# Performance work log

Measured on AMD Instinct MI355X. Metric: run time of the kernel, lower is better.

The kernel has to match this reference:

```python
import jax, jax.numpy as jnp
import numpy as np

N = 50000
E = 800000
D_IN = 128
D_H = 128
D_OUT = 128
EPS = 1e-5


def setup_inputs() -> dict:
    key = jax.random.key(0)
    ks = jax.random.split(key, 16)
    s = 1.0 / np.sqrt(D_IN)
    inp = {
        "x": jax.random.normal(ks[0], (N, D_IN), dtype=jnp.float32),
        "src": jax.random.randint(ks[1], (E,), 0, N, dtype=jnp.int32),
        "dst": jax.random.randint(ks[2], (E,), 0, N, dtype=jnp.int32),
        # SAGEConv layer 1 (in->hidden): fc_self, fc_neigh, bias
        "Ws1": jax.random.uniform(ks[3], (D_IN, D_H), jnp.float32, -s, s),
        "Wn1": jax.random.uniform(ks[4], (D_IN, D_H), jnp.float32, -s, s),
        "b1": jnp.zeros((D_H,), jnp.float32),
        # BN1
        "gamma1": jnp.ones((D_H,), jnp.float32),
        "beta1": jnp.zeros((D_H,), jnp.float32),
        # SAGEConv layer 2 (hidden->hidden)
        "Ws2": jax.random.uniform(ks[5], (D_H, D_H), jnp.float32, -s, s),
        "Wn2": jax.random.uniform(ks[6], (D_H, D_H), jnp.float32, -s, s),
        "b2": jnp.zeros((D_H,), jnp.float32),
        # BN2
        "gamma2": jnp.ones((D_H,), jnp.float32),
        "beta2": jnp.zeros((D_H,), jnp.float32),
        # SAGEConv layer 3 (hidden->out)
        "Ws3": jax.random.uniform(ks[7], (D_H, D_OUT), jnp.float32, -s, s),
        "Wn3": jax.random.uniform(ks[8], (D_H, D_OUT), jnp.float32, -s, s),
        "b3": jnp.zeros((D_OUT,), jnp.float32),
    }
    return inp


def _sage_conv(x, src, dst, Ws, Wn, b):
    # mean aggregation of neighbor (src) features onto dst nodes
    agg = jax.ops.segment_sum(x[src], dst, num_segments=N)  # [N, d]
    deg = jax.ops.segment_sum(jnp.ones((E,), x.dtype), dst, num_segments=N)
    h_neigh = agg / jnp.maximum(deg, 1.0)[:, None]  # isolated nodes -> 0
    return x @ Ws + h_neigh @ Wn + b


def _batch_norm(h, gamma, beta):
    mu = jnp.mean(h, axis=0)
    var = jnp.mean(jnp.square(h - mu), axis=0)  # biased var (torch BN)
    return (h - mu) * jax.lax.rsqrt(var + EPS) * gamma + beta


def reference(x, src, dst, Ws1, Wn1, b1, gamma1, beta1,
              Ws2, Wn2, b2, gamma2, beta2, Ws3, Wn3, b3):
    h = jax.nn.relu(_batch_norm(_sage_conv(x, src, dst, Ws1, Wn1, b1), gamma1, beta1))
    # dropout is identity at inference
    h = jax.nn.relu(_batch_norm(_sage_conv(h, src, dst, Ws2, Wn2, b2), gamma2, beta2))
    return _sage_conv(h, src, dst, Ws3, Wn3, b3)
```

## Files before the change

### kernel.cpp

```cpp
#include <hip/hip_runtime.h>

#define N_NODES 50000
#define NEDGE   800000
#define D       128
#define EPS     1e-5f

typedef __attribute__((ext_vector_type(8))) short bf16x8;
typedef __attribute__((ext_vector_type(4))) float f32x4;
typedef __attribute__((ext_vector_type(8))) unsigned short u16x8;

__device__ inline uint32_t bfhi(float f) {
    uint32_t u = __float_as_uint(f);
    u += 0x7fffu + ((u >> 16) & 1u);
    return u >> 16;
}
__device__ inline float bff(uint32_t h) { return __uint_as_float(h << 16); }

__global__ __launch_bounds__(256) void k_deg(const int* __restrict__ dst,
                                             int* __restrict__ degi) {
    int e = blockIdx.x * 256 + threadIdx.x;
    if (e < NEDGE) atomicAdd(&degi[dst[e]], 1);
}

__global__ __launch_bounds__(256) void k_scan1(const int* __restrict__ degi,
                                               int* __restrict__ offs,
                                               int* __restrict__ bsum) {
    __shared__ int s[256];
    int tid = threadIdx.x;
    int i = blockIdx.x * 256 + tid;
    int v = (i < N_NODES) ? degi[i] : 0;
    s[tid] = v;
    __syncthreads();
    for (int d = 1; d < 256; d <<= 1) {
        int t = (tid >= d) ? s[tid - d] : 0;
        __syncthreads();
        s[tid] += t;
        __syncthreads();
    }
    if (i < N_NODES) offs[i] = s[tid] - v;
    if (tid == 255) bsum[blockIdx.x] = s[255];
}

__global__ __launch_bounds__(256) void k_scan2(int* __restrict__ bsum, int nb) {
    __shared__ int s[256];
    int tid = threadIdx.x;
    int v = (tid < nb) ? bsum[tid] : 0;
    s[tid] = v;
    __syncthreads();
    for (int d = 1; d < 256; d <<= 1) {
        int t = (tid >= d) ? s[tid - d] : 0;
        __syncthreads();
        s[tid] += t;
        __syncthreads();
    }
    if (tid < nb) bsum[tid] = s[tid] - v;
}

__global__ __launch_bounds__(256) void k_scan3(const int* __restrict__ degi,
                                               const int* __restrict__ bsum,
                                               int* __restrict__ offs,
                                               int* __restrict__ cursor,
                                               float* __restrict__ invdeg) {
    int i = blockIdx.x * 256 + threadIdx.x;
    if (i < N_NODES) {
        int o = offs[i] + bsum[blockIdx.x];
        offs[i] = o;
        cursor[i] = o;
        int dg = degi[i];
        invdeg[i] = 1.0f / (float)(dg > 0 ? dg : 1);
    }
    if (i == 0 && blockIdx.x == 0) offs[N_NODES] = NEDGE;
}

__global__ __launch_bounds__(256) void k_fill(const int* __restrict__ src,
                                              const int* __restrict__ dst,
                                              int* __restrict__ cursor,
                                              int* __restrict__ csr) {
    int e = blockIdx.x * 256 + threadIdx.x;
    if (e < NEDGE) {
        int p = atomicAdd(&cursor[dst[e]], 1);
        csr[p] = src[e];
    }
}

__global__ __launch_bounds__(256) void k_tobf16(const float* __restrict__ X,
                                                unsigned short* __restrict__ XB) {
    int t = blockIdx.x * 256 + threadIdx.x;
    if (t >= (N_NODES * D) / 8) return;
    const float* p = X + (size_t)t * 8;
    float4 a = *reinterpret_cast<const float4*>(p);
    float4 b = *reinterpret_cast<const float4*>(p + 4);
    u16x8 o;
    o[0] = (unsigned short)bfhi(a.x); o[1] = (unsigned short)bfhi(a.y);
    o[2] = (unsigned short)bfhi(a.z); o[3] = (unsigned short)bfhi(a.w);
    o[4] = (unsigned short)bfhi(b.x); o[5] = (unsigned short)bfhi(b.y);
    o[6] = (unsigned short)bfhi(b.z); o[7] = (unsigned short)bfhi(b.w);
    *reinterpret_cast<u16x8*>(XB + (size_t)t * 8) = o;
}

__global__ __launch_bounds__(256) void k_agg(const unsigned short* __restrict__ XB,
                                             const int* __restrict__ offs,
                                             const int* __restrict__ csr,
                                             const float* __restrict__ invdeg,
                                             const float* __restrict__ bnscale,
                                             const float* __restrict__ bnshift,
                                             int useBn,
                                             float* __restrict__ HN) {
    int n = blockIdx.x * 16 + (threadIdx.x >> 4);
    if (n >= N_NODES) return;
    int c = (threadIdx.x & 15) * 8;

    float sc[8], sh[8];
    if (useBn) {
        float4 s0 = *reinterpret_cast<const float4*>(bnscale + c);
        float4 s1 = *reinterpret_cast<const float4*>(bnscale + c + 4);
        float4 h0 = *reinterpret_cast<const float4*>(bnshift + c);
        float4 h1 = *reinterpret_cast<const float4*>(bnshift + c + 4);
        sc[0] = s0.x; sc[1] = s0.y; sc[2] = s0.z; sc[3] = s0.w;
        sc[4] = s1.x; sc[5] = s1.y; sc[6] = s1.z; sc[7] = s1.w;
        sh[0] = h0.x; sh[1] = h0.y; sh[2] = h0.z; sh[3] = h0.w;
        sh[4] = h1.x; sh[5] = h1.y; sh[6] = h1.z; sh[7] = h1.w;
    }

    int e0 = offs[n], e1 = offs[n + 1];
    float acc[8];
#pragma unroll
    for (int i = 0; i < 8; ++i) acc[i] = 0.f;

    for (int e = e0; e < e1; ++e) {
        int s = csr[e];
        u16x8 v = *reinterpret_cast<const u16x8*>(XB + (size_t)s * D + c);
        if (useBn) {
#pragma unroll
            for (int i = 0; i < 8; ++i)
                acc[i] += fmaxf(bff((unsigned short)v[i]) * sc[i] + sh[i], 0.f);
        } else {
#pragma unroll
            for (int i = 0; i < 8; ++i)
                acc[i] += bff((unsigned short)v[i]);
        }
    }
    float id = invdeg[n];
    float4 o0 = {acc[0] * id, acc[1] * id, acc[2] * id, acc[3] * id};
    float4 o1 = {acc[4] * id, acc[5] * id, acc[6] * id, acc[7] * id};
    *reinterpret_cast<float4*>(HN + (size_t)n * D + c) = o0;
    *reinterpret_cast<float4*>(HN + (size_t)n * D + c + 4) = o1;
}

__global__ __launch_bounds__(256) void k_wprep(const float* __restrict__ W0,
                                               const float* __restrict__ W1,
                                               const float* __restrict__ W2,
                                               const float* __restrict__ W3,
                                               const float* __restrict__ W4,
                                               const float* __restrict__ W5,
                                               unsigned short* __restrict__ wt) {
    int mat = blockIdx.x >> 6;
    const float* srcs[6] = {W0, W1, W2, W3, W4, W5};
    const float* W = srcs[mat];
    int t = (blockIdx.x & 63) * 256 + threadIdx.x;
    int k = t >> 7;
    int n = t & 127;
    float w = W[k * 128 + n];
    uint32_t h = bfhi(w);
    uint32_t l = bfhi(w - bff(h));
    unsigned short* base = wt + (size_t)mat * 32768;
    base[n * 128 + k] = (unsigned short)h;
    base[16384 + n * 128 + k] = (unsigned short)l;
}

#define LDS_RS 272
#define LDS_PLANE (64 * LDS_RS)
__global__ __launch_bounds__(512) void k_mm(const float* __restrict__ Xf,
                                            const unsigned short* __restrict__ Xhi,
                                            const unsigned short* __restrict__ Xlo,
                                            const float* __restrict__ HN,
                                            const unsigned short* __restrict__ WsT,
                                            const unsigned short* __restrict__ WnT,
                                            const float* __restrict__ bias,
                                            const float* __restrict__ bnscale,
                                            const float* __restrict__ bnshift,
                                            int mode,
                                            float* __restrict__ OUTf,
                                            unsigned short* __restrict__ OUThi,
                                            unsigned short* __restrict__ OUTlo,
                                            int outFp32,
                                            int doStats,
                                            float* __restrict__ sums) {
    __shared__ __align__(16) unsigned char smem[4 * LDS_PLANE];

    const int tid = threadIdx.x;
    const int lane = tid & 63;
    const int wave = tid >> 6;
    const int row0 = blockIdx.x * 64;
    const int mlo = lane & 15;
    const int g = lane >> 4;
    const int col = (wave << 4) + mlo;
    const int kb = g * 8;

    bf16x8 wsh[4], wsl[4], wnh[4], wnl[4];
#pragma unroll
    for (int kc = 0; kc < 4; ++kc) {
        int ko = kc * 32 + kb;
        wsh[kc] = *reinterpret_cast<const bf16x8*>(WsT + (size_t)col * 128 + ko);
        wsl[kc] = *reinterpret_cast<const bf16x8*>(WsT + 16384 + (size_t)col * 128 + ko);
        wnh[kc] = *reinterpret_cast<const bf16x8*>(WnT + (size_t)col * 128 + ko);
        wnl[kc] = *reinterpret_cast<const bf16x8*>(WnT + 16384 + (size_t)col * 128 + ko);
    }

#pragma unroll
    for (int uu = 0; uu < 2; ++uu) {
        int u = tid + uu * 512;
        int r = u >> 4;
        int ks = u & 15;
        int grow = row0 + r;
        float f[8], a[8];
        if (grow < N_NODES) {
            if (mode == 0) {
                const float* xp = Xf + (size_t)grow * D + ks * 8;
                float4 x0 = *reinterpret_cast<const float4*>(xp);
                float4 x1 = *reinterpret_cast<const float4*>(xp + 4);
                f[0] = x0.x; f[1] = x0.y; f[2] = x0.z; f[3] = x0.w;
                f[4] = x1.x; f[5] = x1.y; f[6] = x1.z; f[7] = x1.w;
            } else {
                u16x8 hi = *reinterpret_cast<const u16x8*>(Xhi + (size_t)grow * D + ks * 8);
                u16x8 lo = *reinterpret_cast<const u16x8*>(Xlo + (size_t)grow * D + ks * 8);
                float4 s0 = *reinterpret_cast<const float4*>(bnscale + ks * 8);
                float4 s1 = *reinterpret_cast<const float4*>(bnscale + ks * 8 + 4);
                float4 h0 = *reinterpret_cast<const float4*>(bnshift + ks * 8);
                float4 h1 = *reinterpret_cast<const float4*>(bnshift + ks * 8 + 4);
                float scv[8] = {s0.x, s0.y, s0.z, s0.w, s1.x, s1.y, s1.z, s1.w};
                float shv[8] = {h0.x, h0.y, h0.z, h0.w, h1.x, h1.y, h1.z, h1.w};
#pragma unroll
                for (int i = 0; i < 8; ++i) {
                    float v = bff((unsigned short)hi[i]) + bff((unsigned short)lo[i]);
                    f[i] = fmaxf(v * scv[i] + shv[i], 0.f);
                }
            }
            const float* ap = HN + (size_t)grow * D + ks * 8;
            float4 a0 = *reinterpret_cast<const float4*>(ap);
            float4 a1 = *reinterpret_cast<const float4*>(ap + 4);
            a[0] = a0.x; a[1] = a0.y; a[2] = a0.z; a[3] = a0.w;
            a[4] = a1.x; a[5] = a1.y; a[6] = a1.z; a[7] = a1.w;
        } else {
#pragma unroll
            for (int i = 0; i < 8; ++i) { f[i] = 0.f; a[i] = 0.f; }
        }
        int base = r * LDS_RS + ks * 16;
        uint32_t h8[8];
        int4 vhi, vlo;
#pragma unroll
        for (int i = 0; i < 8; ++i) h8[i] = bfhi(f[i]);
        vhi.x = h8[0] | (h8[1] << 16); vhi.y = h8[2] | (h8[3] << 16);
        vhi.z = h8[4] | (h8[5] << 16); vhi.w = h8[6] | (h8[7] << 16);
        {
            uint32_t l0 = bfhi(f[0] - bff(h8[0])), l1 = bfhi(f[1] - bff(h8[1]));
            uint32_t l2 = bfhi(f[2] - bff(h8[2])), l3 = bfhi(f[3] - bff(h8[3]));
            uint32_t l4 = bfhi(f[4] - bff(h8[4])), l5 = bfhi(f[5] - bff(h8[5]));
            uint32_t l6 = bfhi(f[6] - bff(h8[6])), l7 = bfhi(f[7] - bff(h8[7]));
            vlo.x = l0 | (l1 << 16); vlo.y = l2 | (l3 << 16);
            vlo.z = l4 | (l5 << 16); vlo.w = l6 | (l7 << 16);
        }
        *reinterpret_cast<int4*>(smem + 0 * LDS_PLANE + base) = vhi;
        *reinterpret_cast<int4*>(smem + 1 * LDS_PLANE + base) = vlo;
#pragma unroll
        for (int i = 0; i < 8; ++i) h8[i] = bfhi(a[i]);
        vhi.x = h8[0] | (h8[1] << 16); vhi.y = h8[2] | (h8[3] << 16);
        vhi.z = h8[4] | (h8[5] << 16); vhi.w = h8[6] | (h8[7] << 16);
        {
            uint32_t l0 = bfhi(a[0] - bff(h8[0])), l1 = bfhi(a[1] - bff(h8[1]));
            uint32_t l2 = bfhi(a[2] - bff(h8[2])), l3 = bfhi(a[3] - bff(h8[3]));
            uint32_t l4 = bfhi(a[4] - bff(h8[4])), l5 = bfhi(a[5] - bff(h8[5]));
            uint32_t l6 = bfhi(a[6] - bff(h8[6])), l7 = bfhi(a[7] - bff(h8[7]));
            vlo.x = l0 | (l1 << 16); vlo.y = l2 | (l3 << 16);
            vlo.z = l4 | (l5 << 16); vlo.w = l6 | (l7 << 16);
        }
        *reinterpret_cast<int4*>(smem + 2 * LDS_PLANE + base) = vhi;
        *reinterpret_cast<int4*>(smem + 3 * LDS_PLANE + base) = vlo;
    }
    __syncthreads();

    f32x4 acc[4];
#pragma unroll
    for (int s = 0; s < 4; ++s) acc[s] = (f32x4){0.f, 0.f, 0.f, 0.f};

#pragma unroll
    for (int kc = 0; kc < 4; ++kc) {
        int ksr = kc * 4 + g;
        int ko = ksr * 16;
#pragma unroll
        for (int s = 0; s < 4; ++s) {
            int ad = (s * 16 + mlo) * LDS_RS + ko;
            bf16x8 xh = *reinterpret_cast<const bf16x8*>(smem + 0 * LDS_PLANE + ad);
            bf16x8 xl = *reinterpret_cast<const bf16x8*>(smem + 1 * LDS_PLANE + ad);
            bf16x8 ah = *reinterpret_cast<const bf16x8*>(smem + 2 * LDS_PLANE + ad);
            bf16x8 al = *reinterpret_cast<const bf16x8*>(smem + 3 * LDS_PLANE + ad);
            acc[s] = __builtin_amdgcn_mfma_f32_16x16x32_bf16(xh, wsh[kc], acc[s], 0, 0, 0);
            acc[s] = __builtin_amdgcn_mfma_f32_16x16x32_bf16(xh, wsl[kc], acc[s], 0, 0, 0);
            acc[s] = __builtin_amdgcn_mfma_f32_16x16x32_bf16(xl, wsh[kc], acc[s], 0, 0, 0);
            acc[s] = __builtin_amdgcn_mfma_f32_16x16x32_bf16(ah, wnh[kc], acc[s], 0, 0, 0);
            acc[s] = __builtin_amdgcn_mfma_f32_16x16x32_bf16(ah, wnl[kc], acc[s], 0, 0, 0);
            acc[s] = __builtin_amdgcn_mfma_f32_16x16x32_bf16(al, wnh[kc], acc[s], 0, 0, 0);
        }
    }

    float bcol = bias[col];
    float cs = 0.f, cq = 0.f;
#pragma unroll
    for (int s = 0; s < 4; ++s) {
#pragma unroll
        for (int r = 0; r < 4; ++r) {
            int grow = row0 + s * 16 + g * 4 + r;
            if (grow < N_NODES) {
                float v = acc[s][r] + bcol;
                if (outFp32) {
                    OUTf[(size_t)grow * D + col] = v;
                } else {
                    uint32_t h = bfhi(v);
                    OUThi[(size_t)grow * D + col] = (unsigned short)h;
                    OUTlo[(size_t)grow * D + col] = (unsigned short)bfhi(v - bff(h));
                }
                cs += v; cq += v * v;
            }
        }
    }
    if (doStats) {
        cs += __shfl_xor(cs, 16); cs += __shfl_xor(cs, 32);
        cq += __shfl_xor(cq, 16); cq += __shfl_xor(cq, 32);
        if (lane < 16) {
            atomicAdd(&sums[col], cs);
            atomicAdd(&sums[128 + col], cq);
        }
    }
}

__global__ void k_bnfin(const float* __restrict__ sums,
                        const float* __restrict__ gamma,
                        const float* __restrict__ beta,
                        float* __restrict__ scale,
                        float* __restrict__ shift) {
    int c = threadIdx.x;
    const float invN = 1.0f / (float)N_NODES;
    float mu = sums[c] * invN;
    float var = sums[128 + c] * invN - mu * mu;
    float s = gamma[c] * rsqrtf(var + EPS);
    scale[c] = s;
    shift[c] = beta[c] - mu * s;
}

extern "C" void kernel_launch(void* const* d_in, const int* in_sizes, int n_in,
                              void* d_out, int out_size, void* d_ws, size_t ws_size,
                              hipStream_t stream) {
    const float* x   = (const float*)d_in[0];
    const int*   src = (const int*)d_in[1];
    const int*   dst = (const int*)d_in[2];
    const float* Ws1 = (const float*)d_in[3];
    const float* Wn1 = (const float*)d_in[4];
    const float* b1  = (const float*)d_in[5];
    const float* g1  = (const float*)d_in[6];
    const float* be1 = (const float*)d_in[7];
    const float* Ws2 = (const float*)d_in[8];
    const float* Wn2 = (const float*)d_in[9];
    const float* b2  = (const float*)d_in[10];
    const float* g2  = (const float*)d_in[11];
    const float* be2 = (const float*)d_in[12];
    const float* Ws3 = (const float*)d_in[13];
    const float* Wn3 = (const float*)d_in[14];
    const float* b3  = (const float*)d_in[15];
    float* out = (float*)d_out;

    char* p = (char*)d_ws;
    auto alloc = [&](size_t bytes) -> char* {
        char* r = p;
        p += (bytes + 255) & ~(size_t)255;
        return r;
    };
    float* hn   = (float*)alloc((size_t)N_NODES * D * 4);
    unsigned short* xb   = (unsigned short*)alloc((size_t)N_NODES * D * 2);
    unsigned short* h1hi = (unsigned short*)alloc((size_t)N_NODES * D * 2);
    unsigned short* h1lo = (unsigned short*)alloc((size_t)N_NODES * D * 2);
    unsigned short* h2hi = (unsigned short*)alloc((size_t)N_NODES * D * 2);
    unsigned short* h2lo = (unsigned short*)alloc((size_t)N_NODES * D * 2);
    int*   csr    = (int*)alloc((size_t)NEDGE * 4);
    int*   offs   = (int*)alloc((size_t)(N_NODES + 1) * 4);
    int*   cursor = (int*)alloc((size_t)N_NODES * 4);
    int*   degi   = (int*)alloc((size_t)N_NODES * 4);
    float* invdeg = (float*)alloc((size_t)N_NODES * 4);
    int*   bsum   = (int*)alloc(1024);
    float* sums   = (float*)alloc(256 * 4);
    float* scale  = (float*)alloc(128 * 4);
    float* shift  = (float*)alloc(128 * 4);
    unsigned short* wt = (unsigned short*)alloc((size_t)6 * 32768 * 2);

    const int NB_E = (NEDGE + 255) / 256;
    const int NB_N = (N_NODES + 255) / 256;
    const int NB_A = (N_NODES + 15) / 16;
    const int NB_M = (N_NODES + 63) / 64;
    const int NB_T = (N_NODES * D / 8 + 255) / 256;

    const unsigned short* WsT1 = wt + 0 * 32768;
    const unsigned short* WnT1 = wt + 1 * 32768;
    const unsigned short* WsT2 = wt + 2 * 32768;
    const unsigned short* WnT2 = wt + 3 * 32768;
    const unsigned short* WsT3 = wt + 4 * 32768;
    const unsigned short* WnT3 = wt + 5 * 32768;

    k_wprep<<<384, 256, 0, stream>>>(Ws1, Wn1, Ws2, Wn2, Ws3, Wn3, wt);
    hipMemsetAsync(degi, 0, (size_t)N_NODES * 4, stream);
    k_deg<<<NB_E, 256, 0, stream>>>(dst, degi);
    k_scan1<<<NB_N, 256, 0, stream>>>(degi, offs, bsum);
    k_scan2<<<1, 256, 0, stream>>>(bsum, NB_N);
    k_scan3<<<NB_N, 256, 0, stream>>>(degi, bsum, offs, cursor, invdeg);
    k_fill<<<NB_E, 256, 0, stream>>>(src, dst, cursor, csr);
    k_tobf16<<<NB_T, 256, 0, stream>>>(x, xb);

    k_agg<<<NB_A, 256, 0, stream>>>(xb, offs, csr, invdeg, scale, shift, 0, hn);
    hipMemsetAsync(sums, 0, 256 * 4, stream);
    k_mm<<<NB_M, 512, 0, stream>>>(x, h1hi, h1lo, hn, WsT1, WnT1, b1, scale, shift,
                                   0, out, h1hi, h1lo, 0, 1, sums);
    k_bnfin<<<1, 128, 0, stream>>>(sums, g1, be1, scale, shift);

    k_agg<<<NB_A, 256, 0, stream>>>(h1hi, offs, csr, invdeg, scale, shift, 1, hn);
    hipMemsetAsync(sums, 0, 256 * 4, stream);
    k_mm<<<NB_M, 512, 0, stream>>>(x, h1hi, h1lo, hn, WsT2, WnT2, b2, scale, shift,
                                   1, out, h2hi, h2lo, 0, 1, sums);
    k_bnfin<<<1, 128, 0, stream>>>(sums, g2, be2, scale, shift);

    k_agg<<<NB_A, 256, 0, stream>>>(h2hi, offs, csr, invdeg, scale, shift, 1, hn);
    k_mm<<<NB_M, 512, 0, stream>>>(x, h2hi, h2lo, hn, WsT3, WnT3, b3, scale, shift,
                                   1, out, h1hi, h1lo, 1, 0, sums);
}
```

Measured before the change: 441.0 us.

## Restructure matmul into persistent multi-tile blocks with register prefetch and swizzled LDS

The dense matmul kernel now uses 256-thread blocks that each process three 32-row tiles. Each wave covers two 16-column groups, the weights stay in registers across tiles, and the next tile's global loads are prefetched into registers while the current tile is on the MFMA units. The LDS layout switches from padded rows to an XOR swizzle to avoid bank conflicts. The aggregation loop is also unrolled by two with dual accumulators to keep more gathers in flight. The cost is higher register pressure and extra barriers per tile.

```diff
diff --git a/kernel.cpp b/kernel.cpp
--- a/kernel.cpp
+++ b/kernel.cpp
@@ -4,6 +4,10 @@
 #define NEDGE   800000
 #define D       128
 #define EPS     1e-5f
+#define MTILE   32
+#define TPB_TILES 3
+#define NTILES  1563
+#define NB_MM   521
 
 typedef __attribute__((ext_vector_type(8))) short bf16x8;
 typedef __attribute__((ext_vector_type(4))) float f32x4;
@@ -123,26 +127,47 @@
     }
 
     int e0 = offs[n], e1 = offs[n + 1];
-    float acc[8];
-#pragma unroll
-    for (int i = 0; i < 8; ++i) acc[i] = 0.f;
-
-    for (int e = e0; e < e1; ++e) {
-        int s = csr[e];
-        u16x8 v = *reinterpret_cast<const u16x8*>(XB + (size_t)s * D + c);
+    float a0[8], a1[8];
+#pragma unroll
+    for (int i = 0; i < 8; ++i) { a0[i] = 0.f; a1[i] = 0.f; }
+
+    int e = e0;
+    for (; e + 2 <= e1; e += 2) {
+        int s0i = csr[e], s1i = csr[e + 1];
+        u16x8 v0 = *reinterpret_cast<const u16x8*>(XB + (size_t)s0i * D + c);
+        u16x8 v1 = *reinterpret_cast<const u16x8*>(XB + (size_t)s1i * D + c);
         if (useBn) {
 #pragma unroll
+            for (int i = 0; i < 8; ++i) {
+                a0[i] += fmaxf(bff((unsigned short)v0[i]) * sc[i] + sh[i], 0.f);
+                a1[i] += fmaxf(bff((unsigned short)v1[i]) * sc[i] + sh[i], 0.f);
+            }
+        } else {
+#pragma unroll
+            for (int i = 0; i < 8; ++i) {
+                a0[i] += bff((unsigned short)v0[i]);
+                a1[i] += bff((unsigned short)v1[i]);
+            }
+        }
+    }
+    if (e < e1) {
+        int s0i = csr[e];
+        u16x8 v0 = *reinterpret_cast<const u16x8*>(XB + (size_t)s0i * D + c);
+        if (useBn) {
+#pragma unroll
             for (int i = 0; i < 8; ++i)
-                acc[i] += fmaxf(bff((unsigned short)v[i]) * sc[i] + sh[i], 0.f);
+                a0[i] += fmaxf(bff((unsigned short)v0[i]) * sc[i] + sh[i], 0.f);
         } else {
 #pragma unroll
             for (int i = 0; i < 8; ++i)
-                acc[i] += bff((unsigned short)v[i]);
+                a0[i] += bff((unsigned short)v0[i]);
         }
     }
     float id = invdeg[n];
-    float4 o0 = {acc[0] * id, acc[1] * id, acc[2] * id, acc[3] * id};
-    float4 o1 = {acc[4] * id, acc[5] * id, acc[6] * id, acc[7] * id};
+    float4 o0 = {(a0[0] + a1[0]) * id, (a0[1] + a1[1]) * id,
+                 (a0[2] + a1[2]) * id, (a0[3] + a1[3]) * id};
+    float4 o1 = {(a0[4] + a1[4]) * id, (a0[5] + a1[5]) * id,
+                 (a0[6] + a1[6]) * id, (a0[7] + a1[7]) * id};
     *reinterpret_cast<float4*>(HN + (size_t)n * D + c) = o0;
     *reinterpret_cast<float4*>(HN + (size_t)n * D + c + 4) = o1;
 }
@@ -168,167 +193,222 @@
     base[16384 + n * 128 + k] = (unsigned short)l;
 }
 
-#define LDS_RS 272
-#define LDS_PLANE (64 * LDS_RS)
-__global__ __launch_bounds__(512) void k_mm(const float* __restrict__ Xf,
-                                            const unsigned short* __restrict__ Xhi,
-                                            const unsigned short* __restrict__ Xlo,
-                                            const float* __restrict__ HN,
-                                            const unsigned short* __restrict__ WsT,
-                                            const unsigned short* __restrict__ WnT,
-                                            const float* __restrict__ bias,
-                                            const float* __restrict__ bnscale,
-                                            const float* __restrict__ bnshift,
-                                            int mode,
-                                            float* __restrict__ OUTf,
-                                            unsigned short* __restrict__ OUThi,
-                                            unsigned short* __restrict__ OUTlo,
-                                            int outFp32,
-                                            int doStats,
-                                            float* __restrict__ sums) {
-    __shared__ __align__(16) unsigned char smem[4 * LDS_PLANE];
+__global__ __launch_bounds__(256, 2) void k_mm(const float* __restrict__ Xf,
+                                               const unsigned short* __restrict__ Xhi,
+                                               const unsigned short* __restrict__ Xlo,
+                                               const float* __restrict__ HN,
+                                               const unsigned short* __restrict__ WsT,
+                                               const unsigned short* __restrict__ WnT,
+                                               const float* __restrict__ bias,
+                                               const float* __restrict__ bnscale,
+                                               const float* __restrict__ bnshift,
+                                               int mode,
+                                               float* __restrict__ OUTf,
+                                               unsigned short* __restrict__ OUThi,
+                                               unsigned short* __restrict__ OUTlo,
+                                               int outFp32,
+                                               int doStats,
+                                               float* __restrict__ sums) {
+    __shared__ __align__(16) unsigned char smem[4 * 8192];
 
     const int tid = threadIdx.x;
     const int lane = tid & 63;
     const int wave = tid >> 6;
-    const int row0 = blockIdx.x * 64;
     const int mlo = lane & 15;
     const int g = lane >> 4;
-    const int col = (wave << 4) + mlo;
-    const int kb = g * 8;
-
-    bf16x8 wsh[4], wsl[4], wnh[4], wnl[4];
-#pragma unroll
-    for (int kc = 0; kc < 4; ++kc) {
-        int ko = kc * 32 + kb;
-        wsh[kc] = *reinterpret_cast<const bf16x8*>(WsT + (size_t)col * 128 + ko);
-        wsl[kc] = *reinterpret_cast<const bf16x8*>(WsT + 16384 + (size_t)col * 128 + ko);
-        wnh[kc] = *reinterpret_cast<const bf16x8*>(WnT + (size_t)col * 128 + ko);
-        wnl[kc] = *reinterpret_cast<const bf16x8*>(WnT + 16384 + (size_t)col * 128 + ko);
-    }
-
-#pragma unroll
-    for (int uu = 0; uu < 2; ++uu) {
-        int u = tid + uu * 512;
-        int r = u >> 4;
-        int ks = u & 15;
-        int grow = row0 + r;
-        float f[8], a[8];
-        if (grow < N_NODES) {
+    const int ks = tid & 15;
+    const int srow = tid >> 4;
+
+    bf16x8 wsh[2][4], wsl[2][4], wnh[2][4], wnl[2][4];
+    int colcb[2];
+    float bcol[2];
+#pragma unroll
+    for (int cb = 0; cb < 2; ++cb) {
+        int col = (wave << 5) + (cb << 4) + mlo;
+        colcb[cb] = col;
+        bcol[cb] = bias[col];
+#pragma unroll
+        for (int kc = 0; kc < 4; ++kc) {
+            int ko = kc * 32 + g * 8;
+            wsh[cb][kc] = *reinterpret_cast<const bf16x8*>(WsT + (size_t)col * 128 + ko);
+            wsl[cb][kc] = *reinterpret_cast<const bf16x8*>(WsT + 16384 + (size_t)col * 128 + ko);
+            wnh[cb][kc] = *reinterpret_cast<const bf16x8*>(WnT + (size_t)col * 128 + ko);
+            wnl[cb][kc] = *reinterpret_cast<const bf16x8*>(WnT + 16384 + (size_t)col * 128 + ko);
+        }
+    }
+
+    float sc8[8], sh8[8];
+    if (mode == 1) {
+        float4 s0 = *reinterpret_cast<const float4*>(bnscale + ks * 8);
+        float4 s1 = *reinterpret_cast<const float4*>(bnscale + ks * 8 + 4);
+        float4 h0 = *reinterpret_cast<const float4*>(bnshift + ks * 8);
+        float4 h1 = *reinterpret_cast<const float4*>(bnshift + ks * 8 + 4);
+        sc8[0] = s0.x; sc8[1] = s0.y; sc8[2] = s0.z; sc8[3] = s0.w;
+        sc8[4] = s1.x; sc8[5] = s1.y; sc8[6] = s1.z; sc8[7] = s1.w;
+        sh8[0] = h0.x; sh8[1] = h0.y; sh8[2] = h0.z; sh8[3] = h0.w;
+        sh8[4] = h1.x; sh8[5] = h1.y; sh8[6] = h1.z; sh8[7] = h1.w;
+    }
+
+    float4 rx0[2], rx1[2], rh0[2], rh1[2];
+    u16x8 rhi[2], rlo[2];
+
+    auto stage_load = [&](int t) {
+#pragma unroll
+        for (int uu = 0; uu < 2; ++uu) {
+            int grow = t * MTILE + srow + uu * 16;
+            if (grow < N_NODES) {
+                const float* ap = HN + (size_t)grow * D + ks * 8;
+                rh0[uu] = *reinterpret_cast<const float4*>(ap);
+                rh1[uu] = *reinterpret_cast<const float4*>(ap + 4);
+                if (mode == 0) {
+                    const float* xp = Xf + (size_t)grow * D + ks * 8;
+                    rx0[uu] = *reinterpret_cast<const float4*>(xp);
+                    rx1[uu] = *reinterpret_cast<const float4*>(xp + 4);
+                } else {
+                    rhi[uu] = *reinterpret_cast<const u16x8*>(Xhi + (size_t)grow * D + ks * 8);
+                    rlo[uu] = *reinterpret_cast<const u16x8*>(Xlo + (size_t)grow * D + ks * 8);
+                }
+            } else {
+                float4 z = {0.f, 0.f, 0.f, 0.f};
+                rh0[uu] = z; rh1[uu] = z;
+                if (mode == 0) { rx0[uu] = z; rx1[uu] = z; }
+                else {
+                    u16x8 zu = {0, 0, 0, 0, 0, 0, 0, 0};
+                    rhi[uu] = zu; rlo[uu] = zu;
+                }
+            }
+        }
+    };
+
+    auto stage_write = [&]() {
+#pragma unroll
+        for (int uu = 0; uu < 2; ++uu) {
+            int r = srow + uu * 16;
+            float f[8], a[8];
             if (mode == 0) {
-                const float* xp = Xf + (size_t)grow * D + ks * 8;
-                float4 x0 = *reinterpret_cast<const float4*>(xp);
-                float4 x1 = *reinterpret_cast<const float4*>(xp + 4);
-                f[0] = x0.x; f[1] = x0.y; f[2] = x0.z; f[3] = x0.w;
-                f[4] = x1.x; f[5] = x1.y; f[6] = x1.z; f[7] = x1.w;
+                f[0] = rx0[uu].x; f[1] = rx0[uu].y; f[2] = rx0[uu].z; f[3] = rx0[uu].w;
+                f[4] = rx1[uu].x; f[5] = rx1[uu].y; f[6] = rx1[uu].z; f[7] = rx1[uu].w;
             } else {
-                u16x8 hi = *reinterpret_cast<const u16x8*>(Xhi + (size_t)grow * D + ks * 8);
-                u16x8 lo = *reinterpret_cast<const u16x8*>(Xlo + (size_t)grow * D + ks * 8);
-                float4 s0 = *reinterpret_cast<const float4*>(bnscale + ks * 8);
-                float4 s1 = *reinterpret_cast<const float4*>(bnscale + ks * 8 + 4);
-                float4 h0 = *reinterpret_cast<const float4*>(bnshift + ks * 8);
-                float4 h1 = *reinterpret_cast<const float4*>(bnshift + ks * 8 + 4);
-                float scv[8] = {s0.x, s0.y, s0.z, s0.w, s1.x, s1.y, s1.z, s1.w};
-                float shv[8] = {h0.x, h0.y, h0.z, h0.w, h1.x, h1.y, h1.z, h1.w};
 #pragma unroll
                 for (int i = 0; i < 8; ++i) {
-                    float v = bff((unsigned short)hi[i]) + bff((unsigned short)lo[i]);
-                    f[i] = fmaxf(v * scv[i] + shv[i], 0.f);
+                    float v = bff((unsigned short)rhi[uu][i]) + bff((unsigned short)rlo[uu][i]);
+                    f[i] = fmaxf(v * sc8[i] + sh8[i], 0.f);
                 }
             }
-            const float* ap = HN + (size_t)grow * D + ks * 8;
-            float4 a0 = *reinterpret_cast<const float4*>(ap);
-            float4 a1 = *reinterpret_cast<const float4*>(ap + 4);
-            a[0] = a0.x; a[1] = a0.y; a[2] = a0.z; a[3] = a0.w;
-            a[4] = a1.x; a[5] = a1.y; a[6] = a1.z; a[7] = a1.w;
-        } else {
-#pragma unroll
-            for (int i = 0; i < 8; ++i) { f[i] = 0.f; a[i] = 0.f; }
-        }
-        int base = r * LDS_RS + ks * 16;
-        uint32_t h8[8];
-        int4 vhi, vlo;
-#pragma unroll
-        for (int i = 0; i < 8; ++i) h8[i] = bfhi(f[i]);
-        vhi.x = h8[0] | (h8[1] << 16); vhi.y = h8[2] | (h8[3] << 16);
-        vhi.z = h8[4] | (h8[5] << 16); vhi.w = h8[6] | (h8[7] << 16);
-        {
-            uint32_t l0 = bfhi(f[0] - bff(h8[0])), l1 = bfhi(f[1] - bff(h8[1]));
-            uint32_t l2 = bfhi(f[2] - bff(h8[2])), l3 = bfhi(f[3] - bff(h8[3]));
-            uint32_t l4 = bfhi(f[4] - bff(h8[4])), l5 = bfhi(f[5] - bff(h8[5]));
-            uint32_t l6 = bfhi(f[6] - bff(h8[6])), l7 = bfhi(f[7] - bff(h8[7]));
-            vlo.x = l0 | (l1 << 16); vlo.y = l2 | (l3 << 16);
-            vlo.z = l4 | (l5 << 16); vlo.w = l6 | (l7 << 16);
-        }
-        *reinterpret_cast<int4*>(smem + 0 * LDS_PLANE + base) = vhi;
-        *reinterpret_cast<int4*>(smem + 1 * LDS_PLANE + base) = vlo;
-#pragma unroll
-        for (int i = 0; i < 8; ++i) h8[i] = bfhi(a[i]);
-        vhi.x = h8[0] | (h8[1] << 16); vhi.y = h8[2] | (h8[3] << 16);
-        vhi.z = h8[4] | (h8[5] << 16); vhi.w = h8[6] | (h8[7] << 16);
-        {
-            uint32_t l0 = bfhi(a[0] - bff(h8[0])), l1 = bfhi(a[1] - bff(h8[1]));
-            uint32_t l2 = bfhi(a[2] - bff(h8[2])), l3 = bfhi(a[3] - bff(h8[3]));
-            uint32_t l4 = bfhi(a[4] - bff(h8[4])), l5 = bfhi(a[5] - bff(h8[5]));
-            uint32_t l6 = bfhi(a[6] - bff(h8[6])), l7 = bfhi(a[7] - bff(h8[7]));
-            vlo.x = l0 | (l1 << 16); vlo.y = l2 | (l3 << 16);
-            vlo.z = l4 | (l5 << 16); vlo.w = l6 | (l7 << 16);
-        }
-        *reinterpret_cast<int4*>(smem + 2 * LDS_PLANE + base) = vhi;
-        *reinterpret_cast<int4*>(smem + 3 * LDS_PLANE + base) = vlo;
-    }
+            a[0] = rh0[uu].x; a[1] = rh0[uu].y; a[2] = rh0[uu].z; a[3] = rh0[uu].w;
+            a[4] = rh1[uu].x; a[5] = rh1[uu].y; a[6] = rh1[uu].z; a[7] = rh1[uu].w;
+
+            int base = r * 256 + ((ks * 16) ^ ((r & 7) << 4));
+            uint32_t h8[8];
+            int4 vhi, vlo;
+#pragma unroll
+            for (int i = 0; i < 8; ++i) h8[i] = bfhi(f[i]);
+            vhi.x = h8[0] | (h8[1] << 16); vhi.y = h8[2] | (h8[3] << 16);
+            vhi.z = h8[4] | (h8[5] << 16); vhi.w = h8[6] | (h8[7] << 16);
+            {
+                uint32_t l0 = bfhi(f[0] - bff(h8[0])), l1 = bfhi(f[1] - bff(h8[1]));
+                uint32_t l2 = bfhi(f[2] - bff(h8[2])), l3 = bfhi(f[3] - bff(h8[3]));
+                uint32_t l4 = bfhi(f[4] - bff(h8[4])), l5 = bfhi(f[5] - bff(h8[5]));
+                uint32_t l6 = bfhi(f[6] - bff(h8[6])), l7 = bfhi(f[7] - bff(h8[7]));
+                vlo.x = l0 | (l1 << 16); vlo.y = l2 | (l3 << 16);
+                vlo.z = l4 | (l5 << 16); vlo.w = l6 | (l7 << 16);
+            }
+            *reinterpret_cast<int4*>(smem + 0 * 8192 + base) = vhi;
+            *reinterpret_cast<int4*>(smem + 1 * 8192 + base) = vlo;
+#pragma unroll
+            for (int i = 0; i < 8; ++i) h8[i] = bfhi(a[i]);
+            vhi.x = h8[0] | (h8[1] << 16); vhi.y = h8[2] | (h8[3] << 16);
+            vhi.z = h8[4] | (h8[5] << 16); vhi.w = h8[6] | (h8[7] << 16);
+            {
+                uint32_t l0 = bfhi(a[0] - bff(h8[0])), l1 = bfhi(a[1] - bff(h8[1]));
+                uint32_t l2 = bfhi(a[2] - bff(h8[2])), l3 = bfhi(a[3] - bff(h8[3]));
+                uint32_t l4 = bfhi(a[4] - bff(h8[4])), l5 = bfhi(a[5] - bff(h8[5]));
+                uint32_t l6 = bfhi(a[6] - bff(h8[6])), l7 = bfhi(a[7] - bff(h8[7]));
+                vlo.x = l0 | (l1 << 16); vlo.y = l2 | (l3 << 16);
+                vlo.z = l4 | (l5 << 16); vlo.w = l6 | (l7 << 16);
+            }
+            *reinterpret_cast<int4*>(smem + 2 * 8192 + base) = vhi;
+            *reinterpret_cast<int4*>(smem + 3 * 8192 + base) = vlo;
+        }
+    };
+
+    const int t0 = blockIdx.x * TPB_TILES;
+    float cs[2] = {0.f, 0.f}, cq[2] = {0.f, 0.f};
+
+    stage_load(t0);
+    stage_write();
     __syncthreads();
 
-    f32x4 acc[4];
-#pragma unroll
-    for (int s = 0; s < 4; ++s) acc[s] = (f32x4){0.f, 0.f, 0.f, 0.f};
-
-#pragma unroll
-    for (int kc = 0; kc < 4; ++kc) {
-        int ksr = kc * 4 + g;
-        int ko = ksr * 16;
-#pragma unroll
-        for (int s = 0; s < 4; ++s) {
-            int ad = (s * 16 + mlo) * LDS_RS + ko;
-            bf16x8 xh = *reinterpret_cast<const bf16x8*>(smem + 0 * LDS_PLANE + ad);
-            bf16x8 xl = *reinterpret_cast<const bf16x8*>(smem + 1 * LDS_PLANE + ad);
-            bf16x8 ah = *reinterpret_cast<const bf16x8*>(smem + 2 * LDS_PLANE + ad);
-            bf16x8 al = *reinterpret_cast<const bf16x8*>(smem + 3 * LDS_PLANE + ad);
-            acc[s] = __builtin_amdgcn_mfma_f32_16x16x32_bf16(xh, wsh[kc], acc[s], 0, 0, 0);
-            acc[s] = __builtin_amdgcn_mfma_f32_16x16x32_bf16(xh, wsl[kc], acc[s], 0, 0, 0);
-            acc[s] = __builtin_amdgcn_mfma_f32_16x16x32_bf16(xl, wsh[kc], acc[s], 0, 0, 0);
-            acc[s] = __builtin_amdgcn_mfma_f32_16x16x32_bf16(ah, wnh[kc], acc[s], 0, 0, 0);
-            acc[s] = __builtin_amdgcn_mfma_f32_16x16x32_bf16(ah, wnl[kc], acc[s], 0, 0, 0);
-            acc[s] = __builtin_amdgcn_mfma_f32_16x16x32_bf16(al, wnh[kc], acc[s], 0, 0, 0);
-        }
-    }
-
-    float bcol = bias[col];
-    float cs = 0.f, cq = 0.f;
-#pragma unroll
-    for (int s = 0; s < 4; ++s) {
-#pragma unroll
-        for (int r = 0; r < 4; ++r) {
-            int grow = row0 + s * 16 + g * 4 + r;
-            if (grow < N_NODES) {
-                float v = acc[s][r] + bcol;
-                if (outFp32) {
-                    OUTf[(size_t)grow * D + col] = v;
-                } else {
-                    uint32_t h = bfhi(v);
-                    OUThi[(size_t)grow * D + col] = (unsigned short)h;
-                    OUTlo[(size_t)grow * D + col] = (unsigned short)bfhi(v - bff(h));
+    for (int tt = 0; tt < TPB_TILES; ++tt) {
+        const int row0 = (t0 + tt) * MTILE;
+        if (tt + 1 < TPB_TILES) stage_load(t0 + tt + 1);
+
+        f32x4 acc[2][2];
+#pragma unroll
+        for (int s = 0; s < 2; ++s)
+#pragma unroll
+            for (int cb = 0; cb < 2; ++cb) acc[s][cb] = (f32x4){0.f, 0.f, 0.f, 0.f};
+
+#pragma unroll
+        for (int kc = 0; kc < 4; ++kc) {
+            int ksr = kc * 4 + g;
+            int koff = (ksr * 16) ^ ((mlo & 7) << 4);
+#pragma unroll
+            for (int s = 0; s < 2; ++s) {
+                int ad = (s * 16 + mlo) * 256 + koff;
+                bf16x8 xh = *reinterpret_cast<const bf16x8*>(smem + 0 * 8192 + ad);
+                bf16x8 xl = *reinterpret_cast<const bf16x8*>(smem + 1 * 8192 + ad);
+                bf16x8 ah = *reinterpret_cast<const bf16x8*>(smem + 2 * 8192 + ad);
+                bf16x8 al = *reinterpret_cast<const bf16x8*>(smem + 3 * 8192 + ad);
+#pragma unroll
+                for (int cb = 0; cb < 2; ++cb) {
+                    acc[s][cb] = __builtin_amdgcn_mfma_f32_16x16x32_bf16(xh, wsh[cb][kc], acc[s][cb], 0, 0, 0);
+                    acc[s][cb] = __builtin_amdgcn_mfma_f32_16x16x32_bf16(xh, wsl[cb][kc], acc[s][cb], 0, 0, 0);
+                    acc[s][cb] = __builtin_amdgcn_mfma_f32_16x16x32_bf16(xl, wsh[cb][kc], acc[s][cb], 0, 0, 0);
+                    acc[s][cb] = __builtin_amdgcn_mfma_f32_16x16x32_bf16(ah, wnh[cb][kc], acc[s][cb], 0, 0, 0);
+                    acc[s][cb] = __builtin_amdgcn_mfma_f32_16x16x32_bf16(ah, wnl[cb][kc], acc[s][cb], 0, 0, 0);
+                    acc[s][cb] = __builtin_amdgcn_mfma_f32_16x16x32_bf16(al, wnh[cb][kc], acc[s][cb], 0, 0, 0);
                 }
-                cs += v; cq += v * v;
-            }
-        }
-    }
+            }
+        }
+
+#pragma unroll
+        for (int s = 0; s < 2; ++s)
+#pragma unroll
+            for (int cb = 0; cb < 2; ++cb)
+#pragma unroll
+                for (int r = 0; r < 4; ++r) {
+                    int grow = row0 + s * 16 + g * 4 + r;
+                    if (grow < N_NODES) {
+                        float v = acc[s][cb][r] + bcol[cb];
+                        if (outFp32) {
+                            OUTf[(size_t)grow * D + colcb[cb]] = v;
+                        } else {
+                            uint32_t h = bfhi(v);
+                            OUThi[(size_t)grow * D + colcb[cb]] = (unsigned short)h;
+                            OUTlo[(size_t)grow * D + colcb[cb]] = (unsigned short)bfhi(v - bff(h));
+                        }
+                        cs[cb] += v; cq[cb] += v * v;
+                    }
+                }
+
+        if (tt + 1 < TPB_TILES) {
+            __syncthreads();
+            stage_write();
+            __syncthreads();
+        }
+    }
+
     if (doStats) {
-        cs += __shfl_xor(cs, 16); cs += __shfl_xor(cs, 32);
-        cq += __shfl_xor(cq, 16); cq += __shfl_xor(cq, 32);
-        if (lane < 16) {
-            atomicAdd(&sums[col], cs);
-            atomicAdd(&sums[128 + col], cq);
+#pragma unroll
+        for (int cb = 0; cb < 2; ++cb) {
+            float s = cs[cb], q = cq[cb];
+            s += __shfl_xor(s, 16); s += __shfl_xor(s, 32);
+            q += __shfl_xor(q, 16); q += __shfl_xor(q, 32);
+            if (lane < 16) {
+                atomicAdd(&sums[colcb[cb]], s);
+                atomicAdd(&sums[128 + colcb[cb]], q);
+            }
         }
     }
 }
@@ -394,7 +474,6 @@
     const int NB_E = (NEDGE + 255) / 256;
     const int NB_N = (N_NODES + 255) / 256;
     const int NB_A = (N_NODES + 15) / 16;
-    const int NB_M = (N_NODES + 63) / 64;
     const int NB_T = (N_NODES * D / 8 + 255) / 256;
 
     const unsigned short* WsT1 = wt + 0 * 32768;
@@ -415,17 +494,17 @@
 
     k_agg<<<NB_A, 256, 0, stream>>>(xb, offs, csr, invdeg, scale, shift, 0, hn);
     hipMemsetAsync(sums, 0, 256 * 4, stream);
-    k_mm<<<NB_M, 512, 0, stream>>>(x, h1hi, h1lo, hn, WsT1, WnT1, b1, scale, shift,
-                                   0, out, h1hi, h1lo, 0, 1, sums);
+    k_mm<<<NB_MM, 256, 0, stream>>>(x, h1hi, h1lo, hn, WsT1, WnT1, b1, scale, shift,
+                                    0, out, h1hi, h1lo, 0, 1, sums);
     k_bnfin<<<1, 128, 0, stream>>>(sums, g1, be1, scale, shift);
 
     k_agg<<<NB_A, 256, 0, stream>>>(h1hi, offs, csr, invdeg, scale, shift, 1, hn);
     hipMemsetAsync(sums, 0, 256 * 4, stream);
-    k_mm<<<NB_M, 512, 0, stream>>>(x, h1hi, h1lo, hn, WsT2, WnT2, b2, scale, shift,
-                                   1, out, h2hi, h2lo, 0, 1, sums);
+    k_mm<<<NB_MM, 256, 0, stream>>>(x, h1hi, h1lo, hn, WsT2, WnT2, b2, scale, shift,
+                                    1, out, h2hi, h2lo, 0, 1, sums);
     k_bnfin<<<1, 128, 0, stream>>>(sums, g2, be2, scale, shift);
 
     k_agg<<<NB_A, 256, 0, stream>>>(h2hi, offs, csr, invdeg, scale, shift, 1, hn);
-    k_mm<<<NB_M, 512, 0, stream>>>(x, h2hi, h2lo, hn, WsT3, WnT3, b3, scale, shift,
-                                   1, out, h1hi, h1lo, 1, 0, sums);
-}
+    k_mm<<<NB_MM, 256, 0, stream>>>(x, h2hi, h2lo, hn, WsT3, WnT3, b3, scale, shift,
+                                    1, out, h1hi, h1lo, 1, 0, sums);
+}
```

Measured after the change: 454.0 us. 2.9% more time.
